# Kernel tuning notes

Measured on AMD Instinct MI355X. Metric: run time of the kernel, lower is better.

Reference implementation:

```python
import jax, jax.numpy as jnp
import numpy as np

NEG_SLOPE = 0.2

def _gc(inp, adj, W, b):
    # Kipf GraphConvolution: adj @ (inp @ W) + b
    return adj @ (inp @ W) + b

def _lrelu(x):
    return jnp.where(x >= 0, x, NEG_SLOPE * x)

def setup_inputs() -> dict:
    key = jax.random.key(0)
    ks = jax.random.split(key, 24)
    Nx, Ny, Fx, Fy, D1, C = 8192, 4096, 512, 256, 256, 64
    s = 0.05
    inp = {
        "hx1": jax.random.uniform(ks[0], (Nx, Nx), jnp.float32) / Nx,
        "hx2": jax.random.uniform(ks[1], (Nx, Ny), jnp.float32) / Ny,
        "x0": jax.random.normal(ks[2], (Nx, Fx), jnp.float32),
        "hy1": jax.random.uniform(ks[3], (Ny, Ny), jnp.float32) / Ny,
        "hy2": jax.random.uniform(ks[4], (Ny, Nx), jnp.float32) / Nx,
        "y0": jax.random.normal(ks[5], (Ny, Fy), jnp.float32),
        "alpha": jnp.float32(0.6),
        "beta": jnp.float32(0.4),
        # weights/biases of the 8 GraphConvolution layers
        "Wx1a": jax.random.normal(ks[6], (Fx, D1), jnp.float32) * s,
        "bx1a": jnp.zeros((D1,), jnp.float32),
        "Wx1b": jax.random.normal(ks[7], (Fy, D1), jnp.float32) * s,
        "bx1b": jnp.zeros((D1,), jnp.float32),
        "Wx2a": jax.random.normal(ks[8], (D1, C), jnp.float32) * s,
        "bx2a": jnp.zeros((C,), jnp.float32),
        "Wx2b": jax.random.normal(ks[9], (D1, C), jnp.float32) * s,
        "bx2b": jnp.zeros((C,), jnp.float32),
        "Wy1a": jax.random.normal(ks[10], (Fy, D1), jnp.float32) * s,
        "by1a": jnp.zeros((D1,), jnp.float32),
        "Wy1b": jax.random.normal(ks[11], (Fx, D1), jnp.float32) * s,
        "by1b": jnp.zeros((D1,), jnp.float32),
        "Wy2a": jax.random.normal(ks[12], (D1, C), jnp.float32) * s,
        "by2a": jnp.zeros((C,), jnp.float32),
        "Wy2b": jax.random.normal(ks[13], (D1, C), jnp.float32) * s,
        "by2b": jnp.zeros((C,), jnp.float32),
    }
    return inp

def reference(hx1, hx2, x0, hy1, hy2, y0, alpha, beta,
              Wx1a, bx1a, Wx1b, bx1b, Wx2a, bx2a, Wx2b, bx2b,
              Wy1a, by1a, Wy1b, by1b, Wy2a, by2a, Wy2b, by2b):
    # layer 1
    x1 = _lrelu(_gc(x0, hx1, Wx1a, bx1a) * alpha + _gc(y0, hx2, Wx1b, bx1b) * (1 - alpha))
    y1 = _lrelu(_gc(y0, hy1, Wy1a, by1a) * beta + _gc(x0, hy2, Wy1b, by1b) * (1 - beta))
    # layer 2
    x2 = _lrelu(_gc(x1, hx1, Wx2a, bx2a) * alpha + _gc(y1, hx2, Wx2b, bx2b) * (1 - alpha))
    y_pre = _gc(y1, hy1, Wy2a, by2a) * beta + _gc(x1, hy2, Wy2b, by2b) * (1 - beta)
    y2 = _lrelu(y_pre)
    h_hat = jax.nn.sigmoid(x2 @ y2.T)            # [Nx, Ny]
    x_output = jax.nn.log_softmax(x2, axis=1)    # [Nx, nclass]
    return (h_hat, x_output)
```

## Files before the change

kernel.cpp:

```cpp
#include <hip/hip_runtime.h>

typedef unsigned short u16;
typedef unsigned char u8;
typedef long i64;
typedef __attribute__((ext_vector_type(8))) short bf16x8;
typedef __attribute__((ext_vector_type(4))) float f32x4;
typedef __attribute__((ext_vector_type(8))) u16 u16x8;
typedef __attribute__((ext_vector_type(4))) u16 u16x4;
typedef __attribute__((ext_vector_type(4))) float f4;

#define DEVI static __device__ __forceinline__

DEVI u16 f2b(float f) { __bf16 h = (__bf16)f; return __builtin_bit_cast(u16, h); }
DEVI float b2f(u16 h) { unsigned u = ((unsigned)h) << 16; return __builtin_bit_cast(float, u); }

DEVI int pk8(float a, float b, float c, float d) {
  int w = __builtin_amdgcn_cvt_pk_fp8_f32(a, b, 0, false);
  return __builtin_amdgcn_cvt_pk_fp8_f32(c, d, w, true);
}

DEVI void gload16(const void* g, void* l) {
  __builtin_amdgcn_global_load_lds((const __attribute__((address_space(1))) void*)g,
                                   (__attribute__((address_space(3))) void*)l, 16, 0, 0);
}

__global__ __launch_bounds__(1024)
void gemmF_k(const float* __restrict__ A0, const float* __restrict__ A1,
             const u8* __restrict__ B0, const u8* __restrict__ B1,
             u8* __restrict__ A0f8, u8* __restrict__ A1f8,
             int K0, int K1, int L0, int L1,
             float* __restrict__ Cout, size_t MN)
{
  constexpr int BM = 128, BK = 64;
  constexpr int LDA = 72;
  constexpr int ASZ = BM * LDA;
  constexpr int BSZ = 256 * BK;
  constexpr int BUFSZ = ASZ + BSZ;
  constexpr float SADJ = 8192.f;
  __shared__ __align__(16) u8 lds[4 * BUFSZ];

  const int tid = threadIdx.x, lane = tid & 63, wave = tid >> 6;
  const int wm = (wave >> 2) * 32, wn = (wave & 3) * 64;
  const int lgrp = lane >> 4, lrow = lane & 15;

  const int gy = gridDim.y;
  const int flat = blockIdx.y + gy * blockIdx.z;
  const int nwg = gy * gridDim.z;
  const int swz = (flat & 7) * (nwg >> 3) + (flat >> 3);
  const int m0 = (swz % gy) * BM;
  const int z  = swz / gy;

  const int nt0 = L0 >> 6, NT = nt0 + (L1 >> 6);

  const int r0 = tid >> 4;
  const int cf = (tid & 15) << 2;

  f32x4 acc[2][4];
#pragma unroll
  for (int m = 0; m < 2; ++m)
#pragma unroll
    for (int n = 0; n < 4; ++n) acc[m][n] = (f32x4){0.f, 0.f, 0.f, 0.f};

  f4 rA0[2], rA1[2];

  auto tileinfo = [&](int t, const float*& Ap, const u8*& Bp, u8*& Af8, int& Kj, int& kk) {
    if (t < nt0) { Ap = A0; Bp = B0; Af8 = A0f8; Kj = K0; kk = z * L0 + (t << 6); }
    else         { Ap = A1; Bp = B1; Af8 = A1f8; Kj = K1; kk = z * L1 + ((t - nt0) << 6); }
  };

  auto loadA = [&](int t, f4 (&r)[2]) {
    const float* Ap; const u8* Bp; u8* Af8; int Kj, kk;
    tileinfo(t, Ap, Bp, Af8, Kj, kk);
#pragma unroll
    for (int j = 0; j < 2; ++j) {
      const int rr = j * 64 + r0;
      r[j] = __builtin_nontemporal_load(
          (const f4*)(Ap + (size_t)(m0 + rr) * Kj + kk + cf));
    }
  };

  auto loadB = [&](int t) {
    const float* Ap; const u8* Bp; u8* Af8; int Kj, kk;
    tileinfo(t, Ap, Bp, Af8, Kj, kk);
    u8* sB = &lds[(t & 3) * BUFSZ] + ASZ;
    const int off = tid * 16;
    const int r = off >> 6, c = off & 63;
    gload16(Bp + (size_t)r * Kj + kk + (c ^ (((r >> 1) & 3) << 4)), sB + off);
  };

  auto writeA = [&](int t, f4 (&r)[2]) {
    const float* Ap; const u8* Bp; u8* Af8; int Kj, kk;
    tileinfo(t, Ap, Bp, Af8, Kj, kk);
    u8* sA = &lds[(t & 3) * BUFSZ];
#pragma unroll
    for (int j = 0; j < 2; ++j) {
      const int rr = j * 64 + r0;
      const int pw = pk8(r[j][0] * SADJ, r[j][1] * SADJ, r[j][2] * SADJ, r[j][3] * SADJ);
      *(int*)&sA[rr * LDA + cf] = pw;
      *(int*)(Af8 + (size_t)(m0 + rr) * Kj + kk + cf) = pw;
    }
  };

  auto compute = [&](int t) {
    const u8* sA = &lds[(t & 3) * BUFSZ];
    const u8* sB = sA + ASZ;
#pragma unroll
    for (int ks = 0; ks < 2; ++ks) {
      i64 a[2], b[4];
#pragma unroll
      for (int m = 0; m < 2; ++m) {
        const int r = wm + m * 16 + lrow;
        a[m] = *(const i64*)&sA[r * LDA + ks * 32 + lgrp * 8];
      }
#pragma unroll
      for (int n = 0; n < 4; ++n) {
        const int r = wn + n * 16 + lrow;
        b[n] = *(const i64*)&sB[r * BK + ((ks * 32 + lgrp * 8) ^ (((r >> 1) & 3) << 4))];
      }
#pragma unroll
      for (int m = 0; m < 2; ++m)
#pragma unroll
        for (int n = 0; n < 4; ++n)
          acc[m][n] = __builtin_amdgcn_mfma_f32_16x16x32_fp8_fp8(a[m], b[n], acc[m][n], 0, 0, 0);
    }
  };

  auto step = [&](int t, f4 (&rIn)[2], f4 (&rOut)[2]) {
    const bool has_next = (t + 1 < NT);
    if (has_next) { loadA(t + 1, rOut); loadB(t + 1); }
    if (!has_next)   asm volatile("s_waitcnt vmcnt(0)" ::: "memory");
    else if (t == 0) asm volatile("s_waitcnt vmcnt(3)" ::: "memory");
    else             asm volatile("s_waitcnt vmcnt(5)" ::: "memory");
    writeA(t, rIn);
    asm volatile("s_waitcnt lgkmcnt(0)" ::: "memory");
    asm volatile("s_barrier" ::: "memory");
    compute(t);
  };

  loadA(0, rA0); loadB(0);

  for (int t = 0; t < NT; t += 2) {
    step(t, rA0, rA1);
    step(t + 1, rA1, rA0);
  }

  float* Cp = Cout + (size_t)z * MN;
#pragma unroll
  for (int n = 0; n < 4; ++n) {
    const int c = wn + n * 16 + lrow;
#pragma unroll
    for (int m = 0; m < 2; ++m) {
      const int rb = m0 + wm + m * 16 + lgrp * 4;
#pragma unroll
      for (int q = 0; q < 4; ++q)
        Cp[(size_t)(rb + q) * 256 + c] = acc[m][n][q];
    }
  }
}

template<int BN>
__global__ __launch_bounds__(256)
void gemm8_k(const u8* __restrict__ A0, const u8* __restrict__ A1,
             const u8* __restrict__ B0, const u8* __restrict__ B1,
             int K0, int K1, int L0, int L1,
             float* __restrict__ Cout, int N, size_t MN)
{
  constexpr int BM = 128, BK = 128;
  constexpr int MR = 4, NR = BN / 32;
  constexpr int ASZ = BM * BK, BSZ = BN * BK;
  __shared__ __align__(16) u8 lds[3 * (ASZ + BSZ)];

  const int tid = threadIdx.x, lane = tid & 63, wave = tid >> 6;
  const int wm = (wave >> 1) * 64, wn = (wave & 1) * (BN / 2);
  const int lgrp = lane >> 4, lrow = lane & 15;

  const int gx = gridDim.x, gy = gridDim.y;
  const int flat = blockIdx.x + gx * (blockIdx.y + gy * blockIdx.z);
  const int nwg = gx * gy * gridDim.z;
  const int swz = (flat & 7) * (nwg >> 3) + (flat >> 3);
  const int n0 = (swz % gx) * BN;
  const int m0 = ((swz / gx) % gy) * BM;
  const int z  = swz / (gx * gy);

  const int nt0 = L0 >> 7, NT = nt0 + (L1 >> 7);

  f32x4 acc[MR][NR];
#pragma unroll
  for (int m = 0; m < MR; ++m)
#pragma unroll
    for (int n = 0; n < NR; ++n) acc[m][n] = (f32x4){0.f, 0.f, 0.f, 0.f};

  auto stage = [&](int buf, int t) {
    const u8* Ap; const u8* Bp; int Kj, kk;
    if (t < nt0) { Ap = A0; Bp = B0; Kj = K0; kk = z * L0 + (t << 7); }
    else         { Ap = A1; Bp = B1; Kj = K1; kk = z * L1 + ((t - nt0) << 7); }
    u8* sA = &lds[buf * (ASZ + BSZ)];
    u8* sB = sA + ASZ;
#pragma unroll
    for (int i = 0; i < ASZ / 4096; ++i) {
      const int off = i * 4096 + tid * 16;
      const int r = off >> 7, c = off & 127;
      gload16(Ap + (size_t)(m0 + r) * Kj + kk + (c ^ ((r & 7) << 4)), sA + off);
    }
#pragma unroll
    for (int i = 0; i < BSZ / 4096; ++i) {
      const int off = i * 4096 + tid * 16;
      const int r = off >> 7, c = off & 127;
      gload16(Bp + (size_t)(n0 + r) * Kj + kk + (c ^ ((r & 7) << 4)), sB + off);
    }
  };

  auto compute = [&](int buf) {
    const u8* sA = &lds[buf * (ASZ + BSZ)];
    const u8* sB = sA + ASZ;
#pragma unroll
    for (int ks = 0; ks < 4; ++ks) {
      i64 a[MR], b[NR];
#pragma unroll
      for (int m = 0; m < MR; ++m) {
        const int r = wm + m * 16 + lrow;
        a[m] = *(const i64*)&sA[r * BK + ((ks * 32 + lgrp * 8) ^ ((r & 7) << 4))];
      }
#pragma unroll
      for (int n = 0; n < NR; ++n) {
        const int r = wn + n * 16 + lrow;
        b[n] = *(const i64*)&sB[r * BK + ((ks * 32 + lgrp * 8) ^ ((r & 7) << 4))];
      }
#pragma unroll
      for (int m = 0; m < MR; ++m)
#pragma unroll
        for (int n = 0; n < NR; ++n)
          acc[m][n] = __builtin_amdgcn_mfma_f32_16x16x32_fp8_fp8(a[m], b[n], acc[m][n], 0, 0, 0);
    }
  };

  stage(0, 0);
  stage(1, 1);
  for (int t = 0; t < NT; ++t) {
    if (t + 1 < NT) asm volatile("s_waitcnt vmcnt(6)" ::: "memory");
    else            asm volatile("s_waitcnt vmcnt(0)" ::: "memory");
    asm volatile("s_barrier" ::: "memory");
    compute(t % 3);
    if (t + 2 < NT) stage((t + 2) % 3, t + 2);
  }

  float* Cp = Cout + (size_t)z * MN;
#pragma unroll
  for (int n = 0; n < NR; ++n) {
    const int c = n0 + wn + n * 16 + lrow;
#pragma unroll
    for (int m = 0; m < MR; ++m) {
      const int rb = m0 + wm + m * 16 + lgrp * 4;
#pragma unroll
      for (int q = 0; q < 4; ++q)
        Cp[(size_t)(rb + q) * N + c] = acc[m][n][q];
    }
  }
}

template<int BM, int BN, bool A_F32, int EPI>
__global__ __launch_bounds__(256)
void gemm_k(const void* A0_, const u16* B0_, int K0,
            void* Cout, void* Cout2, int nsplit, int ldc, float sOut)
{
  constexpr int BK = 32;
  constexpr int LD = 40;
  constexpr int MR = BM / 32;
  constexpr int NR = BN / 32;
  __shared__ u16 sA[BM * LD];
  __shared__ u16 sB[BN * LD];

  const int tid  = threadIdx.x;
  const int lane = tid & 63;
  const int wave = tid >> 6;
  const int wm = (wave >> 1) * (BM / 2);
  const int wn = (wave &  1) * (BN / 2);
  const int m0 = blockIdx.y * BM;
  const int n0 = blockIdx.x * BN;

  constexpr int TPRA = 256 / BM;
  constexpr int EPTA = 32 / TPRA;
  constexpr int TPRB = 256 / BN;
  constexpr int EPTB = 32 / TPRB;
  const int ar = tid / TPRA, ac = (tid % TPRA) * EPTA;
  const int br = tid / TPRB, bc = (tid % TPRB) * EPTB;

  f32x4 acc[MR][NR];
#pragma unroll
  for (int m = 0; m < MR; ++m)
#pragma unroll
    for (int n = 0; n < NR; ++n) acc[m][n] = (f32x4){0.f, 0.f, 0.f, 0.f};

  const int lgrp = lane >> 4, lrow = lane & 15;

  for (int kk = 0; kk < K0; kk += BK) {
    if constexpr (A_F32) {
      const float* Ap = (const float*)A0_ + (size_t)(m0 + ar) * K0 + kk + ac;
#pragma unroll
      for (int q = 0; q < EPTA / 8; ++q) {
        f4 v0 = ((const f4*)Ap)[2 * q];
        f4 v1 = ((const f4*)Ap)[2 * q + 1];
        u16x8 h;
        h[0]=f2b(v0[0]); h[1]=f2b(v0[1]); h[2]=f2b(v0[2]); h[3]=f2b(v0[3]);
        h[4]=f2b(v1[0]); h[5]=f2b(v1[1]); h[6]=f2b(v1[2]); h[7]=f2b(v1[3]);
        *(u16x8*)&sA[ar * LD + ac + q * 8] = h;
      }
    } else {
      const u16* Ap = (const u16*)A0_ + (size_t)(m0 + ar) * K0 + kk + ac;
#pragma unroll
      for (int q = 0; q < EPTA / 8; ++q)
        *(u16x8*)&sA[ar * LD + ac + q * 8] = ((const u16x8*)Ap)[q];
    }
    {
      const u16* Bp = B0_ + (size_t)(n0 + br) * K0 + kk + bc;
#pragma unroll
      for (int q = 0; q < EPTB / 8; ++q)
        *(u16x8*)&sB[br * LD + bc + q * 8] = ((const u16x8*)Bp)[q];
    }
    __syncthreads();
    bf16x8 af[MR], bfr[NR];
#pragma unroll
    for (int m = 0; m < MR; ++m)
      af[m] = *(const bf16x8*)&sA[(wm + m * 16 + lrow) * LD + lgrp * 8];
#pragma unroll
    for (int n = 0; n < NR; ++n)
      bfr[n] = *(const bf16x8*)&sB[(wn + n * 16 + lrow) * LD + lgrp * 8];
#pragma unroll
    for (int m = 0; m < MR; ++m)
#pragma unroll
      for (int n = 0; n < NR; ++n)
        acc[m][n] = __builtin_amdgcn_mfma_f32_16x16x32_bf16(af[m], bfr[n], acc[m][n], 0, 0, 0);
    __syncthreads();
  }

  if constexpr (EPI == 2) {
#pragma unroll
    for (int n = 0; n < NR; ++n) {
      const int c = n0 + wn + n * 16 + lrow;
      u8* Cp = (c < nsplit) ? (u8*)Cout : (u8*)Cout2;
      const int cr = (c < nsplit) ? c : c - nsplit;
#pragma unroll
      for (int m = 0; m < MR; ++m) {
        const int rb = m0 + wm + m * 16 + lgrp * 4;
        int w = __builtin_amdgcn_cvt_pk_fp8_f32(acc[m][n][0] * sOut, acc[m][n][1] * sOut, 0, false);
        w = __builtin_amdgcn_cvt_pk_fp8_f32(acc[m][n][2] * sOut, acc[m][n][3] * sOut, w, true);
        *(int*)&Cp[(size_t)cr * ldc + rb] = w;
      }
    }
  } else {
    float* Cp = (float*)Cout;
#pragma unroll
    for (int n = 0; n < NR; ++n) {
      const int c = n0 + wn + n * 16 + lrow;
#pragma unroll
      for (int m = 0; m < MR; ++m) {
        const int rb = m0 + wm + m * 16 + lgrp * 4;
#pragma unroll
        for (int q = 0; q < 4; ++q)
          Cp[(size_t)(rb + q) * ldc + c] = 1.f / (1.f + __expf(-acc[m][n][q]));
      }
    }
  }
}

__global__ __launch_bounds__(256)
void combine_k(const float* __restrict__ parts, int KS, int N, size_t MN,
               const float* b0, const float* b1, const float* mixp, u16* out, float invs)
{
  const float mix = *mixp;
  const size_t stride = (size_t)gridDim.x * 1024;
  for (size_t i = ((size_t)blockIdx.x * 256 + threadIdx.x) * 4; i < MN; i += stride) {
    f4 s = {0.f, 0.f, 0.f, 0.f};
    for (int zz = 0; zz < KS; ++zz)
      s += *(const f4*)&parts[(size_t)zz * MN + i];
    const int c = (int)(i % (size_t)N);
    u16x4 o;
#pragma unroll
    for (int q = 0; q < 4; ++q) {
      float v = s[q] * invs + mix * b0[c + q] + (1.f - mix) * b1[c + q];
      v = v >= 0.f ? v : 0.2f * v;
      o[q] = f2b(v);
    }
    *(u16x4*)&out[i] = o;
  }
}

__global__ __launch_bounds__(256)
void prep_w(const float* Wx1a, const float* Wx1b, const float* Wy1a, const float* Wy1b,
            const float* Wx2a, const float* Wx2b, const float* Wy2a, const float* Wy2b,
            u16* WtX, u16* WtY, u16* W2X, u16* W2Y,
            const float* ap, const float* bp)
{
  const int zz = blockIdx.z;
  const float a = *ap, b = *bp;
  const float* W; u16* O; int K, N, roff; float s;
  switch (zz) {
    case 0: W=Wx1a; O=WtX; K=512; N=256; roff=0;   s=a;      break;
    case 1: W=Wy1b; O=WtX; K=512; N=256; roff=256; s=1.f-b;  break;
    case 2: W=Wx1b; O=WtY; K=256; N=256; roff=0;   s=1.f-a;  break;
    case 3: W=Wy1a; O=WtY; K=256; N=256; roff=256; s=b;      break;
    case 4: W=Wx2a; O=W2X; K=256; N=64;  roff=0;   s=a;      break;
    case 5: W=Wy2b; O=W2X; K=256; N=64;  roff=64;  s=1.f-b;  break;
    case 6: W=Wx2b; O=W2Y; K=256; N=64;  roff=0;   s=1.f-a;  break;
    default:W=Wy2a; O=W2Y; K=256; N=64;  roff=64;  s=b;      break;
  }
  const int total = K * N;
  for (int i = blockIdx.x * 256 + threadIdx.x; i < total; i += gridDim.x * 256) {
    const int k = i / N, n = i - k * N;
    O[(size_t)(n + roff) * K + k] = f2b(W[i] * s);
  }
}

__global__ __launch_bounds__(256)
void softmax_k(const u16* x, float* out)
{
  const int row  = blockIdx.x * 4 + (threadIdx.x >> 6);
  const int lane = threadIdx.x & 63;
  const float v = b2f(x[row * 64 + lane]);
  float m = v;
#pragma unroll
  for (int off = 32; off; off >>= 1) m = fmaxf(m, __shfl_xor(m, off));
  float s = __expf(v - m);
#pragma unroll
  for (int off = 32; off; off >>= 1) s += __shfl_xor(s, off);
  out[(size_t)row * 64 + lane] = v - m - __logf(s);
}

extern "C" void kernel_launch(void* const* d_in, const int* in_sizes, int n_in,
                              void* d_out, int out_size, void* d_ws, size_t ws_size,
                              hipStream_t stream)
{
  const float* hx1 = (const float*)d_in[0];
  const float* hx2 = (const float*)d_in[1];
  const float* x0  = (const float*)d_in[2];
  const float* hy1 = (const float*)d_in[3];
  const float* hy2 = (const float*)d_in[4];
  const float* y0  = (const float*)d_in[5];
  const float* alphap = (const float*)d_in[6];
  const float* betap  = (const float*)d_in[7];
  const float* Wx1a = (const float*)d_in[8];  const float* bx1a = (const float*)d_in[9];
  const float* Wx1b = (const float*)d_in[10]; const float* bx1b = (const float*)d_in[11];
  const float* Wx2a = (const float*)d_in[12]; const float* bx2a = (const float*)d_in[13];
  const float* Wx2b = (const float*)d_in[14]; const float* bx2b = (const float*)d_in[15];
  const float* Wy1a = (const float*)d_in[16]; const float* by1a = (const float*)d_in[17];
  const float* Wy1b = (const float*)d_in[18]; const float* by1b = (const float*)d_in[19];
  const float* Wy2a = (const float*)d_in[20]; const float* by2a = (const float*)d_in[21];
  const float* Wy2b = (const float*)d_in[22]; const float* by2b = (const float*)d_in[23];
  (void)in_sizes; (void)n_in; (void)out_size;

  constexpr int Nx = 8192, Ny = 4096, Fx = 512, Fy = 256, D1 = 256, C = 64;
  constexpr float SB1 = 16.f, SB2 = 256.f;
  constexpr float INV1 = 1.f / (8192.f * 16.f);
  constexpr float INV2 = 1.f / (8192.f * 256.f);
  constexpr int KSx = 4, KSy = 8;

  u8* wsb = (u8*)d_ws;
  size_t off = 0;
  auto alloc = [&](size_t n) { u8* p = wsb + off; off += (n + 63) & ~(size_t)63; return p; };

  u16* WtX = (u16*)alloc((size_t)512 * 512 * 2);
  u16* WtY = (u16*)alloc((size_t)512 * 256 * 2);
  u16* W2X = (u16*)alloc((size_t)128 * 256 * 2);
  u16* W2Y = (u16*)alloc((size_t)128 * 256 * 2);
  u8* B1x  = alloc((size_t)D1 * Nx);
  u8* B2x  = alloc((size_t)D1 * Ny);
  u8* B1y  = alloc((size_t)D1 * Ny);
  u8* B2y  = alloc((size_t)D1 * Nx);
  u16* x1  = (u16*)alloc((size_t)Nx * D1 * 2);
  u16* y1  = (u16*)alloc((size_t)Ny * D1 * 2);
  u8* B1x2 = alloc((size_t)C * Nx);
  u8* B2x2 = alloc((size_t)C * Ny);
  u8* B1y2 = alloc((size_t)C * Ny);
  u8* B2y2 = alloc((size_t)C * Nx);
  u16* x2  = (u16*)alloc((size_t)Nx * C * 2);
  u16* y2  = (u16*)alloc((size_t)Ny * C * 2);

  const size_t base_off = off;
  const size_t szHx1 = (size_t)Nx * Nx, szHx2 = (size_t)Nx * Ny;
  const size_t szHy1 = (size_t)Ny * Ny, szHy2 = (size_t)Ny * Nx;
  const size_t needA = base_off + szHx1 + szHx2 + szHy1 + szHy2 + ((size_t)32 << 20) + (1 << 20);

  u8 *hx1f8, *hx2f8, *hy1f8, *hy2f8; float* part;
  if (ws_size >= needA) {
    hx1f8 = alloc(szHx1); hx2f8 = alloc(szHx2);
    hy1f8 = alloc(szHy1); hy2f8 = alloc(szHy2);
    part  = (float*)alloc((size_t)32 << 20);
  } else {
    hy1f8 = alloc(szHy1); hy2f8 = alloc(szHy2);
    hx1f8 = (u8*)d_out;
    hx2f8 = (u8*)d_out + szHx1;
    part  = (float*)((u8*)d_out + szHx1 + szHx2);
  }

  const size_t MNx1 = (size_t)Nx * D1, MNy1 = (size_t)Ny * D1;
  const size_t MNx2 = (size_t)Nx * C,  MNy2 = (size_t)Ny * C;

  prep_w<<<dim3(256, 1, 8), 256, 0, stream>>>(Wx1a, Wx1b, Wy1a, Wy1b, Wx2a, Wx2b, Wy2a, Wy2b,
      WtX, WtY, W2X, W2Y, alphap, betap);

  gemm_k<64,64,true,2><<<dim3(8, Nx/64), 256, 0, stream>>>(x0, WtX, Fx, B1x, B2y, 256, Nx, SB1);
  gemm_k<64,64,true,2><<<dim3(8, Ny/64), 256, 0, stream>>>(y0, WtY, Fy, B2x, B1y, 256, Ny, SB1);

  gemmF_k<<<dim3(1, Nx/128, KSx), 1024, 0, stream>>>(hx1, hx2, B1x, B2x, hx1f8, hx2f8,
      Nx, Ny, Nx/KSx, Ny/KSx, part, MNx1);
  combine_k<<<dim3(2048), 256, 0, stream>>>(part, KSx, D1, MNx1, bx1a, bx1b, alphap, x1, INV1);
  gemmF_k<<<dim3(1, Ny/128, KSy), 1024, 0, stream>>>(hy1, hy2, B1y, B2y, hy1f8, hy2f8,
      Ny, Nx, Ny/KSy, Nx/KSy, part, MNy1);
  combine_k<<<dim3(1024), 256, 0, stream>>>(part, KSy, D1, MNy1, by1a, by1b, betap, y1, INV1);

  gemm_k<64,64,false,2><<<dim3(2, Nx/64), 256, 0, stream>>>(x1, W2X, D1, B1x2, B2y2, 64, Nx, SB2);
  gemm_k<64,64,false,2><<<dim3(2, Ny/64), 256, 0, stream>>>(y1, W2Y, D1, B2x2, B1y2, 64, Ny, SB2);

  gemm8_k<64><<<dim3(1, 64, 8), 256, 0, stream>>>(hx1f8, hx2f8, B1x2, B2x2, Nx, Ny, 1024, 512, part, C, MNx2);
  combine_k<<<dim3(512), 256, 0, stream>>>(part, 8, C, MNx2, bx2a, bx2b, alphap, x2, INV2);
  gemm8_k<64><<<dim3(1, 32, 16), 256, 0, stream>>>(hy1f8, hy2f8, B1y2, B2y2, Ny, Nx, 256, 512, part, C, MNy2);
  combine_k<<<dim3(256), 256, 0, stream>>>(part, 16, C, MNy2, by2a, by2b, betap, y2, INV2);

  gemm_k<128,128,false,3><<<dim3(Ny/128, Nx/128), 256, 0, stream>>>(x2, y2, C, d_out, nullptr, 0, Ny, 1.f);

  softmax_k<<<dim3(Nx/4), 256, 0, stream>>>(x2, (float*)d_out + (size_t)Nx * Ny);
}
```

Baseline: 360.4 us.

## Merge paired GEMM launches, store split-K partials as bf16, add MFMA priority

The x and y branches of the small weight GEMMs and of the layer-2 fp8 adjacency GEMMs are merged into single launches that pick their operands by block index. Split-K partial sums are now written and read as bf16 instead of fp32, which halves partial-buffer traffic but rounds the partials before they are summed. s_setprio is raised around the MFMA compute loops. The templated gemm_k is split into dedicated specialised kernels.

```diff
diff --git a/kernel.cpp b/kernel.cpp
--- a/kernel.cpp
+++ b/kernel.cpp
@@ -29,7 +29,7 @@
              const u8* __restrict__ B0, const u8* __restrict__ B1,
              u8* __restrict__ A0f8, u8* __restrict__ A1f8,
              int K0, int K1, int L0, int L1,
-             float* __restrict__ Cout, size_t MN)
+             u16* __restrict__ Cout, size_t MN)
 {
   constexpr int BM = 128, BK = 64;
   constexpr int LDA = 72;
@@ -104,6 +104,7 @@
   auto compute = [&](int t) {
     const u8* sA = &lds[(t & 3) * BUFSZ];
     const u8* sB = sA + ASZ;
+    __builtin_amdgcn_s_setprio(1);
 #pragma unroll
     for (int ks = 0; ks < 2; ++ks) {
       i64 a[2], b[4];
@@ -123,6 +124,7 @@
         for (int n = 0; n < 4; ++n)
           acc[m][n] = __builtin_amdgcn_mfma_f32_16x16x32_fp8_fp8(a[m], b[n], acc[m][n], 0, 0, 0);
     }
+    __builtin_amdgcn_s_setprio(0);
   };
 
   auto step = [&](int t, f4 (&rIn)[2], f4 (&rOut)[2]) {
@@ -144,7 +146,7 @@
     step(t + 1, rA1, rA0);
   }
 
-  float* Cp = Cout + (size_t)z * MN;
+  u16* Cp = Cout + (size_t)z * MN;
 #pragma unroll
   for (int n = 0; n < 4; ++n) {
     const int c = wn + n * 16 + lrow;
@@ -153,34 +155,42 @@
       const int rb = m0 + wm + m * 16 + lgrp * 4;
 #pragma unroll
       for (int q = 0; q < 4; ++q)
-        Cp[(size_t)(rb + q) * 256 + c] = acc[m][n][q];
-    }
-  }
-}
-
-template<int BN>
+        Cp[(size_t)(rb + q) * 256 + c] = f2b(acc[m][n][q]);
+    }
+  }
+}
+
 __global__ __launch_bounds__(256)
-void gemm8_k(const u8* __restrict__ A0, const u8* __restrict__ A1,
-             const u8* __restrict__ B0, const u8* __restrict__ B1,
-             int K0, int K1, int L0, int L1,
-             float* __restrict__ Cout, int N, size_t MN)
-{
-  constexpr int BM = 128, BK = 128;
-  constexpr int MR = 4, NR = BN / 32;
+void gemm8_k(const u8* __restrict__ xA0, const u8* __restrict__ xA1,
+             const u8* __restrict__ xB0, const u8* __restrict__ xB1,
+             int xK0, int xK1, int xL0, int xL1, u16* __restrict__ xC, size_t xMN,
+             const u8* __restrict__ yA0, const u8* __restrict__ yA1,
+             const u8* __restrict__ yB0, const u8* __restrict__ yB1,
+             int yK0, int yK1, int yL0, int yL1, u16* __restrict__ yC, size_t yMN)
+{
+  constexpr int BM = 128, BK = 128, BN = 64;
+  constexpr int MR = 4, NR = 2;
   constexpr int ASZ = BM * BK, BSZ = BN * BK;
   __shared__ __align__(16) u8 lds[3 * (ASZ + BSZ)];
 
   const int tid = threadIdx.x, lane = tid & 63, wave = tid >> 6;
-  const int wm = (wave >> 1) * 64, wn = (wave & 1) * (BN / 2);
+  const int wm = (wave >> 1) * 64, wn = (wave & 1) * 32;
   const int lgrp = lane >> 4, lrow = lane & 15;
 
-  const int gx = gridDim.x, gy = gridDim.y;
-  const int flat = blockIdx.x + gx * (blockIdx.y + gy * blockIdx.z);
-  const int nwg = gx * gy * gridDim.z;
+  const int flat = blockIdx.x;
+  const int nwg = gridDim.x;
   const int swz = (flat & 7) * (nwg >> 3) + (flat >> 3);
-  const int n0 = (swz % gx) * BN;
-  const int m0 = ((swz / gx) % gy) * BM;
-  const int z  = swz / (gx * gy);
+
+  const u8 *A0, *A1, *B0, *B1; int K0, K1, L0, L1; u16* Cw; size_t MN;
+  int m0, z;
+  if (swz < 512) {
+    A0=xA0; A1=xA1; B0=xB0; B1=xB1; K0=xK0; K1=xK1; L0=xL0; L1=xL1; Cw=xC; MN=xMN;
+    m0 = (swz & 63) * BM; z = swz >> 6;
+  } else {
+    const int id = swz - 512;
+    A0=yA0; A1=yA1; B0=yB0; B1=yB1; K0=yK0; K1=yK1; L0=yL0; L1=yL1; Cw=yC; MN=yMN;
+    m0 = (id & 31) * BM; z = id >> 5;
+  }
 
   const int nt0 = L0 >> 7, NT = nt0 + (L1 >> 7);
 
@@ -206,13 +216,14 @@
     for (int i = 0; i < BSZ / 4096; ++i) {
       const int off = i * 4096 + tid * 16;
       const int r = off >> 7, c = off & 127;
-      gload16(Bp + (size_t)(n0 + r) * Kj + kk + (c ^ ((r & 7) << 4)), sB + off);
+      gload16(Bp + (size_t)r * Kj + kk + (c ^ ((r & 7) << 4)), sB + off);
     }
   };
 
   auto compute = [&](int buf) {
     const u8* sA = &lds[buf * (ASZ + BSZ)];
     const u8* sB = sA + ASZ;
+    __builtin_amdgcn_s_setprio(1);
 #pragma unroll
     for (int ks = 0; ks < 4; ++ks) {
       i64 a[MR], b[NR];
@@ -232,6 +243,7 @@
         for (int n = 0; n < NR; ++n)
           acc[m][n] = __builtin_amdgcn_mfma_f32_16x16x32_fp8_fp8(a[m], b[n], acc[m][n], 0, 0, 0);
     }
+    __builtin_amdgcn_s_setprio(0);
   };
 
   stage(0, 0);
@@ -244,46 +256,51 @@
     if (t + 2 < NT) stage((t + 2) % 3, t + 2);
   }
 
-  float* Cp = Cout + (size_t)z * MN;
+  u16* Cp = Cw + (size_t)z * MN;
 #pragma unroll
   for (int n = 0; n < NR; ++n) {
-    const int c = n0 + wn + n * 16 + lrow;
+    const int c = wn + n * 16 + lrow;
 #pragma unroll
     for (int m = 0; m < MR; ++m) {
       const int rb = m0 + wm + m * 16 + lgrp * 4;
 #pragma unroll
       for (int q = 0; q < 4; ++q)
-        Cp[(size_t)(rb + q) * N + c] = acc[m][n][q];
-    }
-  }
-}
-
-template<int BM, int BN, bool A_F32, int EPI>
+        Cp[(size_t)(rb + q) * 64 + c] = f2b(acc[m][n][q]);
+    }
+  }
+}
+
+template<bool A_F32>
 __global__ __launch_bounds__(256)
-void gemm_k(const void* A0_, const u16* B0_, int K0,
-            void* Cout, void* Cout2, int nsplit, int ldc, float sOut)
-{
-  constexpr int BK = 32;
-  constexpr int LD = 40;
-  constexpr int MR = BM / 32;
-  constexpr int NR = BN / 32;
+void gemmS_k(const void* Ax, const u16* Bx, int Kx, int ldcx, u8* Cx1, u8* Cx2,
+             const void* Ay, const u16* By, int Ky, int ldcy, u8* Cy1, u8* Cy2,
+             int ySplit, int nsplit, float sOut)
+{
+  constexpr int BM = 64, BN = 64, BK = 32, LD = 40;
+  constexpr int MR = 2, NR = 2;
   __shared__ u16 sA[BM * LD];
   __shared__ u16 sB[BN * LD];
 
   const int tid  = threadIdx.x;
   const int lane = tid & 63;
   const int wave = tid >> 6;
-  const int wm = (wave >> 1) * (BM / 2);
-  const int wn = (wave &  1) * (BN / 2);
-  const int m0 = blockIdx.y * BM;
+  const int wm = (wave >> 1) * 32;
+  const int wn = (wave &  1) * 32;
+
+  const void* A0_; const u16* B0_; int K0, ldc; u8 *C1, *C2; int m0;
+  if ((int)blockIdx.y < ySplit) {
+    A0_ = Ax; B0_ = Bx; K0 = Kx; ldc = ldcx; C1 = Cx1; C2 = Cx2;
+    m0 = blockIdx.y * BM;
+  } else {
+    A0_ = Ay; B0_ = By; K0 = Ky; ldc = ldcy; C1 = Cy1; C2 = Cy2;
+    m0 = (blockIdx.y - ySplit) * BM;
+  }
   const int n0 = blockIdx.x * BN;
 
   constexpr int TPRA = 256 / BM;
   constexpr int EPTA = 32 / TPRA;
-  constexpr int TPRB = 256 / BN;
-  constexpr int EPTB = 32 / TPRB;
   const int ar = tid / TPRA, ac = (tid % TPRA) * EPTA;
-  const int br = tid / TPRB, bc = (tid % TPRB) * EPTB;
+  const int br = ar, bc = ac;
 
   f32x4 acc[MR][NR];
 #pragma unroll
@@ -296,26 +313,19 @@
   for (int kk = 0; kk < K0; kk += BK) {
     if constexpr (A_F32) {
       const float* Ap = (const float*)A0_ + (size_t)(m0 + ar) * K0 + kk + ac;
-#pragma unroll
-      for (int q = 0; q < EPTA / 8; ++q) {
-        f4 v0 = ((const f4*)Ap)[2 * q];
-        f4 v1 = ((const f4*)Ap)[2 * q + 1];
-        u16x8 h;
-        h[0]=f2b(v0[0]); h[1]=f2b(v0[1]); h[2]=f2b(v0[2]); h[3]=f2b(v0[3]);
-        h[4]=f2b(v1[0]); h[5]=f2b(v1[1]); h[6]=f2b(v1[2]); h[7]=f2b(v1[3]);
-        *(u16x8*)&sA[ar * LD + ac + q * 8] = h;
-      }
+      f4 v0 = ((const f4*)Ap)[0];
+      f4 v1 = ((const f4*)Ap)[1];
+      u16x8 h;
+      h[0]=f2b(v0[0]); h[1]=f2b(v0[1]); h[2]=f2b(v0[2]); h[3]=f2b(v0[3]);
+      h[4]=f2b(v1[0]); h[5]=f2b(v1[1]); h[6]=f2b(v1[2]); h[7]=f2b(v1[3]);
+      *(u16x8*)&sA[ar * LD + ac] = h;
     } else {
       const u16* Ap = (const u16*)A0_ + (size_t)(m0 + ar) * K0 + kk + ac;
-#pragma unroll
-      for (int q = 0; q < EPTA / 8; ++q)
-        *(u16x8*)&sA[ar * LD + ac + q * 8] = ((const u16x8*)Ap)[q];
+      *(u16x8*)&sA[ar * LD + ac] = *(const u16x8*)Ap;
     }
     {
       const u16* Bp = B0_ + (size_t)(n0 + br) * K0 + kk + bc;
-#pragma unroll
-      for (int q = 0; q < EPTB / 8; ++q)
-        *(u16x8*)&sB[br * LD + bc + q * 8] = ((const u16x8*)Bp)[q];
+      *(u16x8*)&sB[br * LD + bc] = *(const u16x8*)Bp;
     }
     __syncthreads();
     bf16x8 af[MR], bfr[NR];
@@ -333,46 +343,101 @@
     __syncthreads();
   }
 
-  if constexpr (EPI == 2) {
-#pragma unroll
-    for (int n = 0; n < NR; ++n) {
-      const int c = n0 + wn + n * 16 + lrow;
-      u8* Cp = (c < nsplit) ? (u8*)Cout : (u8*)Cout2;
-      const int cr = (c < nsplit) ? c : c - nsplit;
-#pragma unroll
-      for (int m = 0; m < MR; ++m) {
-        const int rb = m0 + wm + m * 16 + lgrp * 4;
-        int w = __builtin_amdgcn_cvt_pk_fp8_f32(acc[m][n][0] * sOut, acc[m][n][1] * sOut, 0, false);
-        w = __builtin_amdgcn_cvt_pk_fp8_f32(acc[m][n][2] * sOut, acc[m][n][3] * sOut, w, true);
-        *(int*)&Cp[(size_t)cr * ldc + rb] = w;
-      }
-    }
-  } else {
-    float* Cp = (float*)Cout;
-#pragma unroll
-    for (int n = 0; n < NR; ++n) {
-      const int c = n0 + wn + n * 16 + lrow;
-#pragma unroll
-      for (int m = 0; m < MR; ++m) {
-        const int rb = m0 + wm + m * 16 + lgrp * 4;
-#pragma unroll
-        for (int q = 0; q < 4; ++q)
-          Cp[(size_t)(rb + q) * ldc + c] = 1.f / (1.f + __expf(-acc[m][n][q]));
-      }
+#pragma unroll
+  for (int n = 0; n < NR; ++n) {
+    const int c = n0 + wn + n * 16 + lrow;
+    u8* Cp = (c < nsplit) ? C1 : C2;
+    const int cr = (c < nsplit) ? c : c - nsplit;
+#pragma unroll
+    for (int m = 0; m < MR; ++m) {
+      const int rb = m0 + wm + m * 16 + lgrp * 4;
+      int w = __builtin_amdgcn_cvt_pk_fp8_f32(acc[m][n][0] * sOut, acc[m][n][1] * sOut, 0, false);
+      w = __builtin_amdgcn_cvt_pk_fp8_f32(acc[m][n][2] * sOut, acc[m][n][3] * sOut, w, true);
+      *(int*)&Cp[(size_t)cr * ldc + rb] = w;
     }
   }
 }
 
 __global__ __launch_bounds__(256)
-void combine_k(const float* __restrict__ parts, int KS, int N, size_t MN,
+void gemmH_k(const u16* A0_, const u16* B0_, int K0, float* Cout, int ldc)
+{
+  constexpr int BM = 128, BN = 128, BK = 32, LD = 40;
+  constexpr int MR = 4, NR = 4;
+  __shared__ u16 sA[BM * LD];
+  __shared__ u16 sB[BN * LD];
+
+  const int tid  = threadIdx.x;
+  const int lane = tid & 63;
+  const int wave = tid >> 6;
+  const int wm = (wave >> 1) * 64;
+  const int wn = (wave &  1) * 64;
+  const int m0 = blockIdx.y * BM;
+  const int n0 = blockIdx.x * BN;
+
+  constexpr int TPRA = 2;
+  constexpr int EPTA = 16;
+  const int ar = tid / TPRA, ac = (tid % TPRA) * EPTA;
+
+  f32x4 acc[MR][NR];
+#pragma unroll
+  for (int m = 0; m < MR; ++m)
+#pragma unroll
+    for (int n = 0; n < NR; ++n) acc[m][n] = (f32x4){0.f, 0.f, 0.f, 0.f};
+
+  const int lgrp = lane >> 4, lrow = lane & 15;
+
+  for (int kk = 0; kk < K0; kk += BK) {
+    {
+      const u16* Ap = A0_ + (size_t)(m0 + ar) * K0 + kk + ac;
+      *(u16x8*)&sA[ar * LD + ac]     = ((const u16x8*)Ap)[0];
+      *(u16x8*)&sA[ar * LD + ac + 8] = ((const u16x8*)Ap)[1];
+      const u16* Bp = B0_ + (size_t)(n0 + ar) * K0 + kk + ac;
+      *(u16x8*)&sB[ar * LD + ac]     = ((const u16x8*)Bp)[0];
+      *(u16x8*)&sB[ar * LD + ac + 8] = ((const u16x8*)Bp)[1];
+    }
+    __syncthreads();
+    bf16x8 af[MR], bfr[NR];
+#pragma unroll
+    for (int m = 0; m < MR; ++m)
+      af[m] = *(const bf16x8*)&sA[(wm + m * 16 + lrow) * LD + lgrp * 8];
+#pragma unroll
+    for (int n = 0; n < NR; ++n)
+      bfr[n] = *(const bf16x8*)&sB[(wn + n * 16 + lrow) * LD + lgrp * 8];
+#pragma unroll
+    for (int m = 0; m < MR; ++m)
+#pragma unroll
+      for (int n = 0; n < NR; ++n)
+        acc[m][n] = __builtin_amdgcn_mfma_f32_16x16x32_bf16(af[m], bfr[n], acc[m][n], 0, 0, 0);
+    __syncthreads();
+  }
+
+  float* Cp = Cout;
+#pragma unroll
+  for (int n = 0; n < NR; ++n) {
+    const int c = n0 + wn + n * 16 + lrow;
+#pragma unroll
+    for (int m = 0; m < MR; ++m) {
+      const int rb = m0 + wm + m * 16 + lgrp * 4;
+#pragma unroll
+      for (int q = 0; q < 4; ++q)
+        Cp[(size_t)(rb + q) * ldc + c] = 1.f / (1.f + __expf(-acc[m][n][q]));
+    }
+  }
+}
+
+__global__ __launch_bounds__(256)
+void combine_k(const u16* __restrict__ parts, int KS, int N, size_t MN,
                const float* b0, const float* b1, const float* mixp, u16* out, float invs)
 {
   const float mix = *mixp;
   const size_t stride = (size_t)gridDim.x * 1024;
   for (size_t i = ((size_t)blockIdx.x * 256 + threadIdx.x) * 4; i < MN; i += stride) {
     f4 s = {0.f, 0.f, 0.f, 0.f};
-    for (int zz = 0; zz < KS; ++zz)
-      s += *(const f4*)&parts[(size_t)zz * MN + i];
+    for (int zz = 0; zz < KS; ++zz) {
+      u16x4 pv = *(const u16x4*)&parts[(size_t)zz * MN + i];
+#pragma unroll
+      for (int q = 0; q < 4; ++q) s[q] += b2f(pv[q]);
+    }
     const int c = (int)(i % (size_t)N);
     u16x4 o;
 #pragma unroll
@@ -480,16 +545,16 @@
   const size_t szHy1 = (size_t)Ny * Ny, szHy2 = (size_t)Ny * Nx;
   const size_t needA = base_off + szHx1 + szHx2 + szHy1 + szHy2 + ((size_t)32 << 20) + (1 << 20);
 
-  u8 *hx1f8, *hx2f8, *hy1f8, *hy2f8; float* part;
+  u8 *hx1f8, *hx2f8, *hy1f8, *hy2f8; u16* part;
   if (ws_size >= needA) {
     hx1f8 = alloc(szHx1); hx2f8 = alloc(szHx2);
     hy1f8 = alloc(szHy1); hy2f8 = alloc(szHy2);
-    part  = (float*)alloc((size_t)32 << 20);
+    part  = (u16*)alloc((size_t)32 << 20);
   } else {
     hy1f8 = alloc(szHy1); hy2f8 = alloc(szHy2);
     hx1f8 = (u8*)d_out;
     hx2f8 = (u8*)d_out + szHx1;
-    part  = (float*)((u8*)d_out + szHx1 + szHx2);
+    part  = (u16*)((u8*)d_out + szHx1 + szHx2);
   }
 
   const size_t MNx1 = (size_t)Nx * D1, MNy1 = (size_t)Ny * D1;
@@ -498,8 +563,10 @@
   prep_w<<<dim3(256, 1, 8), 256, 0, stream>>>(Wx1a, Wx1b, Wy1a, Wy1b, Wx2a, Wx2b, Wy2a, Wy2b,
       WtX, WtY, W2X, W2Y, alphap, betap);
 
-  gemm_k<64,64,true,2><<<dim3(8, Nx/64), 256, 0, stream>>>(x0, WtX, Fx, B1x, B2y, 256, Nx, SB1);
-  gemm_k<64,64,true,2><<<dim3(8, Ny/64), 256, 0, stream>>>(y0, WtY, Fy, B2x, B1y, 256, Ny, SB1);
+  gemmS_k<true><<<dim3(8, Nx/64 + Ny/64), 256, 0, stream>>>(
+      x0, WtX, Fx, Nx, B1x, B2y,
+      y0, WtY, Fy, Ny, B2x, B1y,
+      Nx/64, 256, SB1);
 
   gemmF_k<<<dim3(1, Nx/128, KSx), 1024, 0, stream>>>(hx1, hx2, B1x, B2x, hx1f8, hx2f8,
       Nx, Ny, Nx/KSx, Ny/KSx, part, MNx1);
@@ -508,15 +575,19 @@
       Ny, Nx, Ny/KSy, Nx/KSy, part, MNy1);
   combine_k<<<dim3(1024), 256, 0, stream>>>(part, KSy, D1, MNy1, by1a, by1b, betap, y1, INV1);
 
-  gemm_k<64,64,false,2><<<dim3(2, Nx/64), 256, 0, stream>>>(x1, W2X, D1, B1x2, B2y2, 64, Nx, SB2);
-  gemm_k<64,64,false,2><<<dim3(2, Ny/64), 256, 0, stream>>>(y1, W2Y, D1, B2x2, B1y2, 64, Ny, SB2);
-
-  gemm8_k<64><<<dim3(1, 64, 8), 256, 0, stream>>>(hx1f8, hx2f8, B1x2, B2x2, Nx, Ny, 1024, 512, part, C, MNx2);
+  gemmS_k<false><<<dim3(2, Nx/64 + Ny/64), 256, 0, stream>>>(
+      x1, W2X, D1, Nx, B1x2, B2y2,
+      y1, W2Y, D1, Ny, B2x2, B1y2,
+      Nx/64, 64, SB2);
+
+  u16* partY2 = part + 8 * MNx2;
+  gemm8_k<<<dim3(1024), 256, 0, stream>>>(
+      hx1f8, hx2f8, B1x2, B2x2, Nx, Ny, 1024, 512, part, MNx2,
+      hy1f8, hy2f8, B1y2, B2y2, Ny, Nx, 256, 512, partY2, MNy2);
   combine_k<<<dim3(512), 256, 0, stream>>>(part, 8, C, MNx2, bx2a, bx2b, alphap, x2, INV2);
-  gemm8_k<64><<<dim3(1, 32, 16), 256, 0, stream>>>(hy1f8, hy2f8, B1y2, B2y2, Ny, Nx, 256, 512, part, C, MNy2);
-  combine_k<<<dim3(256), 256, 0, stream>>>(part, 16, C, MNy2, by2a, by2b, betap, y2, INV2);
-
-  gemm_k<128,128,false,3><<<dim3(Ny/128, Nx/128), 256, 0, stream>>>(x2, y2, C, d_out, nullptr, 0, Ny, 1.f);
+  combine_k<<<dim3(256), 256, 0, stream>>>(partY2, 16, C, MNy2, by2a, by2b, betap, y2, INV2);
+
+  gemmH_k<<<dim3(Ny/128, Nx/128), 256, 0, stream>>>(x2, y2, C, (float*)d_out, Ny);
 
   softmax_k<<<dim3(Nx/4), 256, 0, stream>>>(x2, (float*)d_out + (size_t)Nx * Ny);
 }
```

After: 345.0 us. -4.3%, faster.
